# Performance work log

Measured on AMD Instinct MI355X. Metric: run time of the kernel, lower is better.

The kernel has to match this reference:

```python
import jax, jax.numpy as jnp
import numpy as np

B, S, H, KV, D, HID = 1, 2048, 32, 8, 128, 4096
SCALE = D ** -0.5
EPS = 1e-5
QMAX = 127.0  # 8-bit symmetric fake quant


def fake_quant(x):
    # per-tensor symmetric int8 fake quantization with straight-through estimator
    s = jnp.maximum(jnp.max(jnp.abs(x)), 1e-5) / QMAX
    q = jnp.clip(jnp.round(x / s), -QMAX - 1.0, QMAX) * s
    return x + jax.lax.stop_gradient(q - x)


def rms_norm(x, w):
    xf = x.astype(jnp.float32)
    var = jnp.mean(xf * xf, axis=-1, keepdims=True)
    return (xf * jax.lax.rsqrt(var + EPS)).astype(x.dtype) * w


def rotate_half(x):
    h = x.shape[-1] // 2
    return jnp.concatenate([-x[..., h:], x[..., :h]], axis=-1)


def qlinear(x, W):
    # QuantLinear: fake-quant activation and weight, then matmul (no bias)
    return fake_quant(x) @ fake_quant(W).T


def setup_inputs() -> dict:
    key = jax.random.key(0)
    ks = jax.random.split(key, 5)
    hidden_states = jax.random.normal(ks[0], (B, S, HID), jnp.float32)
    # RoPE tables
    inv_freq = 1.0 / (10000.0 ** (np.arange(0, D, 2, dtype=np.float32) / D))
    freqs = np.outer(np.arange(S, dtype=np.float32), inv_freq)  # [S, D/2]
    emb = np.concatenate([freqs, freqs], axis=-1)  # [S, D]
    cos = jnp.asarray(np.cos(emb))[None]  # [1,S,D]
    sin = jnp.asarray(np.sin(emb))[None]
    # causal additive mask [1,1,S,S]
    mask = jnp.where(np.tril(np.ones((S, S), dtype=bool)), 0.0, -1e9).astype(jnp.float32)[None, None]
    Wq = jax.random.normal(ks[1], (H * D, HID), jnp.float32) * 0.02
    Wk = jax.random.normal(ks[2], (KV * D, HID), jnp.float32) * 0.02
    Wv = jax.random.normal(ks[3], (KV * D, HID), jnp.float32) * 0.02
    Wo = jax.random.normal(ks[4], (HID, H * D), jnp.float32) * 0.02
    q_norm_w = jnp.ones((D,), jnp.float32)
    k_norm_w = jnp.ones((D,), jnp.float32)
    return dict(hidden_states=hidden_states, cos=cos, sin=sin, attention_mask=mask,
                Wq=Wq, Wk=Wk, Wv=Wv, Wo=Wo, q_norm_w=q_norm_w, k_norm_w=k_norm_w)


def reference(hidden_states, cos, sin, attention_mask, Wq, Wk, Wv, Wo, q_norm_w, k_norm_w):
    b, s, _ = hidden_states.shape
    q = qlinear(hidden_states, Wq).reshape(b, s, H, D).transpose(0, 2, 1, 3)   # [B,H,S,D]
    k = qlinear(hidden_states, Wk).reshape(b, s, KV, D).transpose(0, 2, 1, 3)  # [B,KV,S,D]
    v = qlinear(hidden_states, Wv).reshape(b, s, KV, D).transpose(0, 2, 1, 3)
    q = rms_norm(q, q_norm_w)
    k = rms_norm(k, k_norm_w)
    c = cos[:, None]  # unsqueeze head dim -> [1,1,S,D]
    sn = sin[:, None]
    q = q * c + rotate_half(q) * sn
    k = k * c + rotate_half(k) * sn
    n_rep = H // KV
    k = jnp.repeat(k, n_rep, axis=1)  # [B,H,S,D]
    v = jnp.repeat(v, n_rep, axis=1)
    # fake-quant around QK^T
    q = fake_quant(q)
    k = fake_quant(k)
    scores = jnp.einsum('bhqd,bhkd->bhqk', q, k) * SCALE + attention_mask
    p = jax.nn.softmax(scores.astype(jnp.float32), axis=-1).astype(q.dtype)
    # fake-quant around PV
    p = fake_quant(p)
    v = fake_quant(v)
    out = jnp.einsum('bhqk,bhkd->bhqd', p, v)
    out = out.transpose(0, 2, 1, 3).reshape(b, s, H * D)
    return qlinear(out, Wo)
```

## Files before the change

kernel.cpp:

```cpp
#include <hip/hip_runtime.h>
#include <hip/hip_bf16.h>
#include <math.h>
#include <stdint.h>

#define S_LEN 2048
#define NH    32
#define NKV   8
#define HD    128
#define HIDD  4096

typedef unsigned short u16;
typedef __attribute__((ext_vector_type(4))) int i32x4;

#define GLD16(g, l) __builtin_amdgcn_global_load_lds( \
    (const __attribute__((address_space(1))) void*)(g), \
    (__attribute__((address_space(3))) void*)(l), 16, 0, 0)


__device__ __forceinline__ float slot_scale(const unsigned* slot) {
    return fmaxf(__uint_as_float(*slot), 1e-5f) / 127.0f;
}

__device__ __forceinline__ int qint(float x, float s) {
    float q = rintf(x / s);
    q = fminf(fmaxf(q, -128.0f), 127.0f);
    return (int)q;
}

__device__ __forceinline__ void block_amax_atomic(float m, unsigned* slot) {
    __shared__ float wmax[8];
    const int lane = threadIdx.x & 63;
    const int wid  = threadIdx.x >> 6;
    const int nw   = blockDim.x >> 6;
    #pragma unroll
    for (int o = 32; o; o >>= 1) m = fmaxf(m, __shfl_xor(m, o));
    if (lane == 0) wmax[wid] = m;
    __syncthreads();
    if (threadIdx.x == 0) {
        float bm = wmax[0];
        for (int i = 1; i < nw; ++i) bm = fmaxf(bm, wmax[i]);
        atomicMax(slot, __float_as_uint(bm));
    }
}

struct Amax5Args { const float* p[5]; size_t n4[5]; };
__global__ __launch_bounds__(256) void absmax5_kernel(Amax5Args a, unsigned* slots) {
    const int t = blockIdx.y;
    const float4* x4 = (const float4*)a.p[t];
    const size_t n4 = a.n4[t];
    size_t i = (size_t)blockIdx.x * blockDim.x + threadIdx.x;
    size_t stride = (size_t)gridDim.x * blockDim.x;
    float m = 0.0f;
    for (; i < n4; i += stride) {
        float4 v = x4[i];
        m = fmaxf(m, fmaxf(fmaxf(fabsf(v.x), fabsf(v.y)), fmaxf(fabsf(v.z), fabsf(v.w))));
    }
    block_amax_atomic(m, slots + t);
}

struct Quant5Args { const float* p[5]; char* o[5]; size_t n4[5]; };
__global__ __launch_bounds__(256) void quant5_kernel(Quant5Args a, const unsigned* slots) {
    const int t = blockIdx.y;
    float s = slot_scale(slots + t);
    const float4* x4 = (const float4*)a.p[t];
    unsigned* o4 = (unsigned*)a.o[t];
    const size_t n4 = a.n4[t];
    size_t i = (size_t)blockIdx.x * blockDim.x + threadIdx.x;
    size_t stride = (size_t)gridDim.x * blockDim.x;
    for (; i < n4; i += stride) {
        float4 v = x4[i];
        unsigned o = (unsigned)(qint(v.x, s) & 255)
                   | ((unsigned)(qint(v.y, s) & 255) << 8)
                   | ((unsigned)(qint(v.z, s) & 255) << 16)
                   | ((unsigned)(qint(v.w, s) & 255) << 24);
        o4[i] = o;
    }
}

__global__ __launch_bounds__(256) void quant_kernel(const float* __restrict__ x,
                                                    size_t n4, const unsigned* slot,
                                                    char* __restrict__ out) {
    float s = slot_scale(slot);
    size_t i = (size_t)blockIdx.x * blockDim.x + threadIdx.x;
    size_t stride = (size_t)gridDim.x * blockDim.x;
    const float4* x4 = (const float4*)x;
    unsigned* o4 = (unsigned*)out;
    for (; i < n4; i += stride) {
        float4 v = x4[i];
        unsigned o = (unsigned)(qint(v.x, s) & 255)
                   | ((unsigned)(qint(v.y, s) & 255) << 8)
                   | ((unsigned)(qint(v.z, s) & 255) << 16)
                   | ((unsigned)(qint(v.w, s) & 255) << 24);
        o4[i] = o;
    }
}

__device__ __forceinline__ void gemm_body(const char* __restrict__ A,
                                          const char* __restrict__ B,
                                          float* __restrict__ C,
                                          int m0, int n0, int N, int K,
                                          float scale, unsigned* out_amax,
                                          char* Asm, char* Bsm) {
    const int tid  = threadIdx.x;
    const int lane = tid & 63;
    const int wave = tid >> 6;
    const int wr = (wave >> 1) * 64;
    const int wc = (wave & 1) * 64;
    const int l15 = lane & 15;
    const int l4  = lane >> 4;

    i32x4 acc[4][4];
    #pragma unroll
    for (int i = 0; i < 4; ++i)
        #pragma unroll
        for (int j = 0; j < 4; ++j) acc[i][j] = (i32x4){0, 0, 0, 0};

    for (int k0 = 0; k0 < K; k0 += 128) {
        __syncthreads();
        #pragma unroll
        for (int i = 0; i < 4; ++i) {
            int c2  = i * 256 + tid;
            int kk  = i >> 1;
            int row = (c2 >> 2) & 127;
            int col = (c2 & 3) * 16;
            GLD16(&A[(size_t)(m0 + row) * K + k0 + kk * 64 + col], &Asm[i * 4096 + wave * 1024]);
            GLD16(&B[(size_t)(n0 + row) * K + k0 + kk * 64 + col], &Bsm[i * 4096 + wave * 1024]);
        }
        __syncthreads();
        #pragma unroll
        for (int kk = 0; kk < 2; ++kk) {
            i32x4 af[4], bfr[4];
            #pragma unroll
            for (int i = 0; i < 4; ++i)
                af[i] = *(const i32x4*)&Asm[kk * 8192 + (wr + i * 16 + l15) * 64 + l4 * 16];
            #pragma unroll
            for (int j = 0; j < 4; ++j)
                bfr[j] = *(const i32x4*)&Bsm[kk * 8192 + (wc + j * 16 + l15) * 64 + l4 * 16];
            #pragma unroll
            for (int i = 0; i < 4; ++i)
                #pragma unroll
                for (int j = 0; j < 4; ++j)
                    acc[i][j] = __builtin_amdgcn_mfma_i32_16x16x64_i8(af[i], bfr[j], acc[i][j], 0, 0, 0);
        }
    }

    float lm = 0.0f;
    #pragma unroll
    for (int i = 0; i < 4; ++i)
        #pragma unroll
        for (int j = 0; j < 4; ++j)
            #pragma unroll
            for (int r = 0; r < 4; ++r) {
                int row = m0 + wr + i * 16 + l4 * 4 + r;
                int col = n0 + wc + j * 16 + l15;
                float v = (float)acc[i][j][r] * scale;
                C[(size_t)row * N + col] = v;
                lm = fmaxf(lm, fabsf(v));
            }
    if (out_amax) block_amax_atomic(lm, out_amax);
}

__global__ __launch_bounds__(256) void gemm_bt_kernel(const char* __restrict__ A,
                                                      const char* __restrict__ B,
                                                      float* __restrict__ C,
                                                      int N, int K,
                                                      const unsigned* __restrict__ sA_slot,
                                                      const unsigned* __restrict__ sB_slot,
                                                      unsigned* out_amax) {
    __shared__ __align__(16) char Asm[2 * 128 * 64];
    __shared__ __align__(16) char Bsm[2 * 128 * 64];
    int bid = blockIdx.y * 16 + blockIdx.x;
    int swz = (bid & 7) * 64 + (bid >> 3);
    float scale = slot_scale(sA_slot) * slot_scale(sB_slot);
    gemm_body(A, B, C, (swz & 15) * 128, (swz >> 4) * 128, N, K, scale, out_amax, Asm, Bsm);
}

__global__ __launch_bounds__(256) void gemm_kv_kernel(const char* __restrict__ A,
                                                      const char* __restrict__ Bk,
                                                      const char* __restrict__ Bv,
                                                      float* __restrict__ Ck,
                                                      float* __restrict__ Cv,
                                                      int K,
                                                      const unsigned* __restrict__ sA_slot,
                                                      const unsigned* __restrict__ sK_slot,
                                                      const unsigned* __restrict__ sV_slot,
                                                      unsigned* v_amax) {
    __shared__ __align__(16) char Asm[2 * 128 * 64];
    __shared__ __align__(16) char Bsm[2 * 128 * 64];
    int bid = blockIdx.y * 16 + blockIdx.x;
    int swz = (bid & 7) * 32 + (bid >> 3);
    int sx = swz & 15, sy = swz >> 4;
    const bool isv = sy >= 8;
    const char* B = isv ? Bv : Bk;
    float*      C = isv ? Cv : Ck;
    float scale = slot_scale(sA_slot) * slot_scale(isv ? sV_slot : sK_slot);
    gemm_body(A, B, C, sx * 128, (sy & 7) * 128, NKV * HD, K, scale,
              isv ? v_amax : nullptr, Asm, Bsm);
}

__global__ __launch_bounds__(256) void rmsrope2_kernel(float* __restrict__ qx,
                                                       float* __restrict__ kx,
                                                       const float* __restrict__ cosb,
                                                       const float* __restrict__ sinb,
                                                       const float* __restrict__ qw,
                                                       const float* __restrict__ kw,
                                                       unsigned* slots) {
    const int which = blockIdx.y;
    float* x = which ? kx : qx;
    const float* w = which ? kw : qw;
    const int s_shift = which ? 3 : 5;
    const int nrows = which ? (S_LEN * NKV) : (S_LEN * NH);
    unsigned* slot = slots + (which ? 6 : 5);

    const int lane = threadIdx.x & 63;
    const int wid  = threadIdx.x >> 6;
    const float wa = w[lane];
    const float wb = w[lane + 64];
    float lm = 0.0f;
    for (int row = blockIdx.x * 4 + wid; row < nrows; row += gridDim.x * 4) {
        int s = row >> s_shift;
        float* xr = x + (size_t)row * 128;
        float a = xr[lane], b = xr[lane + 64];
        float ss = a * a + b * b;
        #pragma unroll
        for (int o = 32; o; o >>= 1) ss += __shfl_xor(ss, o);
        float inv = 1.0f / sqrtf(ss * (1.0f / 128.0f) + 1e-5f);
        float ya = (a * inv) * wa;
        float yb = (b * inv) * wb;
        const float* cr = cosb + (size_t)s * 128;
        const float* sr = sinb + (size_t)s * 128;
        float o0 = ya * cr[lane]      - yb * sr[lane];
        float o1 = yb * cr[lane + 64] + ya * sr[lane + 64];
        xr[lane] = o0;
        xr[lane + 64] = o1;
        lm = fmaxf(lm, fmaxf(fabsf(o0), fabsf(o1)));
    }
    block_amax_atomic(lm, slot);
}

__global__ __launch_bounds__(256) void quant_qk2_kernel(const float* __restrict__ qx,
                                                        const float* __restrict__ kx,
                                                        const unsigned* slots,
                                                        char* __restrict__ qq,
                                                        char* __restrict__ kq) {
    int tid = blockIdx.x * 256 + threadIdx.x;
    const int qtot = S_LEN * NH * HD;
    if (tid < qtot) {
        float s = slot_scale(slots + 5);
        int d  = tid & 127;
        int h  = (tid >> 7) & 31;
        int sp = tid >> 12;
        qq[((size_t)h * S_LEN + sp) * 128 + d] = (char)qint(qx[tid], s);
    } else {
        tid -= qtot;
        float s = slot_scale(slots + 6);
        int d  = tid & 127;
        int h  = (tid >> 7) & 7;
        int sp = tid >> 10;
        kq[((size_t)h * S_LEN + sp) * 128 + d] = (char)qint(kx[tid], s);
    }
}

__global__ __launch_bounds__(256) void quant_v_kernel(const float* __restrict__ x,
                                                      const unsigned* slot,
                                                      char* __restrict__ out) {
    __shared__ unsigned char t8[64][36];
    const float s = slot_scale(slot);
    const int t   = threadIdx.x;
    const int sp0 = blockIdx.x * 64;
    const int d0  = blockIdx.y * 32;
    const int kvh = blockIdx.z;
    const int dl = t & 31;
    const int sb = t >> 5;
    #pragma unroll
    for (int j = 0; j < 8; ++j) {
        int spl = sb + j * 8;
        float v = x[((size_t)(sp0 + spl) * NKV + kvh) * 128 + d0 + dl];
        t8[spl][dl] = (unsigned char)qint(v, s);
    }
    __syncthreads();
    const int dd = t >> 3;
    const int ch = t & 7;
    unsigned lo = 0, hi = 0;
    #pragma unroll
    for (int j = 0; j < 4; ++j) lo |= (unsigned)t8[ch * 8 + j][dd] << (8 * j);
    #pragma unroll
    for (int j = 0; j < 4; ++j) hi |= (unsigned)t8[ch * 8 + 4 + j][dd] << (8 * j);
    *(uint2*)&out[((size_t)kvh * 128 + d0 + dd) * S_LEN + sp0 + ch * 8] = make_uint2(lo, hi);
}

__global__ __launch_bounds__(256) void attn_kernel(const char* __restrict__ Qq,
                                                   const char* __restrict__ Kq,
                                                   const char* __restrict__ Vt,
                                                   const unsigned* sq_slot,
                                                   const unsigned* sk_slot,
                                                   const unsigned* sv_slot,
                                                   float* __restrict__ O,
                                                   unsigned* amax_slot) {
    __shared__ __align__(16) char Klds[64 * 144];
    __shared__ __align__(16) char Vlds[128 * 80];
    __shared__ __align__(16) char plds[4][16 * 80];

    const int tid  = threadIdx.x;
    const int lane = tid & 63;
    const int wave = tid >> 6;
    const int h  = blockIdx.y;
    const int kv = h >> 2;
    const int l15 = lane & 15;
    const int l4  = lane >> 4;
    const size_t kvS = (size_t)kv * S_LEN;

    const float sq = slot_scale(sq_slot);
    const float sk = slot_scale(sk_slot);
    const float sv = slot_scale(sv_slot);
    const float qk_scale = sq * sk * 0.08838834764831845f;
    const float osc = (1.0f / 127.0f) * sv;
    const float NEG = -1e30f;

    float lm = 0.0f;

    #pragma unroll 1
    for (int tpass = 0; tpass < 2; ++tpass) {
        const int qt  = tpass ? (31 - (int)blockIdx.x) : (int)blockIdx.x;
        const int qr0 = qt * 64 + wave * 16;
        const int kb_last = qt * 4 + wave;
        const int nchunk  = qt + 1;

        i32x4 qf2[2];
        {
            const char* qp = Qq + ((size_t)h * S_LEN + qr0 + l15) * 128 + l4 * 16;
            qf2[0] = *(const i32x4*)(qp);
            qf2[1] = *(const i32x4*)(qp + 64);
        }

        float m_l = NEG, l_l = 0.0f;
        i32x4 kreg[2];
        #pragma unroll
        for (int c = 0; c < 2; ++c) {
            int idx = c * 256 + tid;
            kreg[c] = *(const i32x4*)&Kq[(kvS + (idx >> 3)) * 128 + (idx & 7) * 16];
        }
        #pragma unroll 1
        for (int kc = 0; kc < nchunk; ++kc) {
            __syncthreads();
            #pragma unroll
            for (int c = 0; c < 2; ++c) {
                int idx = c * 256 + tid;
                *(i32x4*)&Klds[(idx >> 3) * 144 + (idx & 7) * 16] = kreg[c];
            }
            __syncthreads();
            if (kc + 1 < nchunk) {
                #pragma unroll
                for (int c = 0; c < 2; ++c) {
                    int idx = c * 256 + tid;
                    kreg[c] = *(const i32x4*)&Kq[(kvS + (kc + 1) * 64 + (idx >> 3)) * 128 + (idx & 7) * 16];
                }
            }
            #pragma unroll
            for (int hb = 0; hb < 4; ++hb) {
                int kb = kc * 4 + hb;
                if (kb > kb_last) continue;
                i32x4 sacc = {0, 0, 0, 0};
                #pragma unroll
                for (int c = 0; c < 2; ++c) {
                    i32x4 kfa = *(const i32x4*)&Klds[(hb * 16 + l15) * 144 + c * 64 + l4 * 16];
                    sacc = __builtin_amdgcn_mfma_i32_16x16x64_i8(kfa, qf2[c], sacc, 0, 0, 0);
                }
                const bool diagb = (kb == kb_last);
                float sc[4];
                float bm = NEG;
                #pragma unroll
                for (int r = 0; r < 4; ++r) {
                    float x = (float)sacc[r] * qk_scale;
                    bool msk = diagb && ((l4 * 4 + r) > l15);
                    sc[r] = x;
                    bm = fmaxf(bm, msk ? NEG : x);
                }
                float mn = fmaxf(m_l, bm);
                float corr = __expf(m_l - mn);
                float ps = 0.0f;
                #pragma unroll
                for (int r = 0; r < 4; ++r) {
                    bool msk = diagb && ((l4 * 4 + r) > l15);
                    float p = msk ? 0.0f : __expf(sc[r] - mn);
                    ps += p;
                }
                l_l = l_l * corr + ps;
                m_l = mn;
            }
        }
        float m2 = fmaxf(m_l, __shfl_xor(m_l, 16));
        float mfin = fmaxf(m2, __shfl_xor(m2, 32));
        float t = l_l * __expf(m_l - mfin);
        t += __shfl_xor(t, 16);
        t += __shfl_xor(t, 32);
        float rl = 127.0f / t;
        float mrowB[4], rlB[4];
        #pragma unroll
        for (int r = 0; r < 4; ++r) {
            mrowB[r] = __shfl(mfin, l4 * 4 + r);
            rlB[r]   = __shfl(rl,   l4 * 4 + r);
        }

        i32x4 oacc[8];
        #pragma unroll
        for (int dt = 0; dt < 8; ++dt) oacc[dt] = (i32x4){0, 0, 0, 0};

        i32x4 vreg[2];
        #pragma unroll
        for (int c = 0; c < 2; ++c) {
            int idx = c * 256 + tid;
            kreg[c] = *(const i32x4*)&Kq[(kvS + (idx >> 3)) * 128 + (idx & 7) * 16];
            vreg[c] = *(const i32x4*)&Vt[((size_t)kv * 128 + (idx >> 2)) * S_LEN + (idx & 3) * 16];
        }
        #pragma unroll 1
        for (int kc = 0; kc < nchunk; ++kc) {
            __syncthreads();
            #pragma unroll
            for (int c = 0; c < 2; ++c) {
                int idx = c * 256 + tid;
                *(i32x4*)&Klds[(idx >> 3) * 144 + (idx & 7) * 16] = kreg[c];
                *(i32x4*)&Vlds[(idx >> 2) * 80 + (idx & 3) * 16] = vreg[c];
            }
            __syncthreads();
            if (kc + 1 < nchunk) {
                #pragma unroll
                for (int c = 0; c < 2; ++c) {
                    int idx = c * 256 + tid;
                    kreg[c] = *(const i32x4*)&Kq[(kvS + (kc + 1) * 64 + (idx >> 3)) * 128 + (idx & 7) * 16];
                    vreg[c] = *(const i32x4*)&Vt[((size_t)kv * 128 + (idx >> 2)) * S_LEN + (kc + 1) * 64 + (idx & 3) * 16];
                }
            }
            #pragma unroll
            for (int hb = 0; hb < 4; ++hb) {
                int kb = kc * 4 + hb;
                unsigned char pz[4] = {0, 0, 0, 0};
                if (kb <= kb_last) {
                    i32x4 sacc = {0, 0, 0, 0};
                    #pragma unroll
                    for (int c = 0; c < 2; ++c) {
                        i32x4 kfb = *(const i32x4*)&Klds[(hb * 16 + l15) * 144 + c * 64 + l4 * 16];
                        sacc = __builtin_amdgcn_mfma_i32_16x16x64_i8(qf2[c], kfb, sacc, 0, 0, 0);
                    }
                    const bool diagb = (kb == kb_last);
                    #pragma unroll
                    for (int r = 0; r < 4; ++r) {
                        float x = (float)sacc[r] * qk_scale;
                        float p = __expf(x - mrowB[r]) * rlB[r];
                        float pq = (diagb && (l15 > l4 * 4 + r)) ? 0.0f : rintf(p);
                        pz[r] = (unsigned char)(int)pq;
                    }
                }
                #pragma unroll
                for (int r = 0; r < 4; ++r)
                    plds[wave][(l4 * 4 + r) * 80 + hb * 16 + l15] = pz[r];
            }
            i32x4 pf = *(const i32x4*)&plds[wave][l15 * 80 + l4 * 16];
            #pragma unroll
            for (int dt = 0; dt < 8; ++dt) {
                i32x4 vfb = *(const i32x4*)&Vlds[(dt * 16 + l15) * 80 + l4 * 16];
                oacc[dt] = __builtin_amdgcn_mfma_i32_16x16x64_i8(pf, vfb, oacc[dt], 0, 0, 0);
            }
        }

        #pragma unroll
        for (int dt = 0; dt < 8; ++dt)
            #pragma unroll
            for (int r = 0; r < 4; ++r) {
                int qrow = qr0 + l4 * 4 + r;
                float v = (float)oacc[dt][r] * osc;
                O[(size_t)qrow * (NH * 128) + h * 128 + dt * 16 + l15] = v;
                lm = fmaxf(lm, fabsf(v));
            }
    }
    block_amax_atomic(lm, amax_slot);
}

extern "C" void kernel_launch(void* const* d_in, const int* in_sizes, int n_in,
                              void* d_out, int out_size, void* d_ws, size_t ws_size,
                              hipStream_t stream) {
    const float* hs   = (const float*)d_in[0];
    const float* cosb = (const float*)d_in[1];
    const float* sinb = (const float*)d_in[2];
    const float* Wq   = (const float*)d_in[4];
    const float* Wk   = (const float*)d_in[5];
    const float* Wv   = (const float*)d_in[6];
    const float* Wo   = (const float*)d_in[7];
    const float* qnw  = (const float*)d_in[8];
    const float* knw  = (const float*)d_in[9];
    float* out = (float*)d_out;

    char* ws = (char*)d_ws;
    unsigned* slots = (unsigned*)ws;
    size_t off = 256;
    auto take = [&](size_t bytes) { size_t o = off; off += (bytes + 255) & ~(size_t)255; return o; };
    char*  hsq  = (char*)(ws + take((size_t)S_LEN * HIDD));
    char*  Wqq  = (char*)(ws + take((size_t)NH * HD * HIDD));
    char*  Wkq  = (char*)(ws + take((size_t)NKV * HD * HIDD));
    char*  Wvq  = (char*)(ws + take((size_t)NKV * HD * HIDD));
    char*  Woq  = (char*)(ws + take((size_t)HIDD * NH * HD));
    float* qf   = (float*)(ws + take((size_t)S_LEN * NH * HD * 4));
    float* kf   = (float*)(ws + take((size_t)S_LEN * NKV * HD * 4));
    float* vf   = (float*)(ws + take((size_t)S_LEN * NKV * HD * 4));
    char*  qq   = (char*)(ws + take((size_t)NH * S_LEN * HD));
    char*  kq   = (char*)(ws + take((size_t)NKV * S_LEN * HD));
    char*  vtq  = (char*)(ws + take((size_t)NKV * HD * S_LEN));
    float* attnf = qf;
    char*  attnq = hsq;

    hipMemsetAsync(ws, 0, 64, stream);

    const size_t n_hs = (size_t)S_LEN * HIDD;
    const size_t n_wq = (size_t)NH * HD * HIDD;
    const size_t n_wk = (size_t)NKV * HD * HIDD;

    Amax5Args aa;
    aa.p[0] = hs; aa.p[1] = Wq; aa.p[2] = Wk; aa.p[3] = Wv; aa.p[4] = Wo;
    aa.n4[0] = n_hs / 4; aa.n4[1] = n_wq / 4; aa.n4[2] = n_wk / 4;
    aa.n4[3] = n_wk / 4; aa.n4[4] = n_wq / 4;
    absmax5_kernel<<<dim3(512, 5), 256, 0, stream>>>(aa, slots);

    Quant5Args qa;
    qa.p[0] = hs; qa.p[1] = Wq; qa.p[2] = Wk; qa.p[3] = Wv; qa.p[4] = Wo;
    qa.o[0] = hsq; qa.o[1] = Wqq; qa.o[2] = Wkq; qa.o[3] = Wvq; qa.o[4] = Woq;
    qa.n4[0] = n_hs / 4; qa.n4[1] = n_wq / 4; qa.n4[2] = n_wk / 4;
    qa.n4[3] = n_wk / 4; qa.n4[4] = n_wq / 4;
    quant5_kernel<<<dim3(1024, 5), 256, 0, stream>>>(qa, slots);

    gemm_bt_kernel<<<dim3(16, 32), 256, 0, stream>>>(hsq, Wqq, qf, NH * HD, HIDD,
                                                     slots + 0, slots + 1, nullptr);
    gemm_kv_kernel<<<dim3(16, 16), 256, 0, stream>>>(hsq, Wkq, Wvq, kf, vf, HIDD,
                                                     slots + 0, slots + 2, slots + 3, slots + 7);

    rmsrope2_kernel<<<dim3(1024, 2), 256, 0, stream>>>(qf, kf, cosb, sinb, qnw, knw, slots);

    quant_qk2_kernel<<<40960, 256, 0, stream>>>(qf, kf, slots, qq, kq);
    quant_v_kernel<<<dim3(32, 4, 8), 256, 0, stream>>>(vf, slots + 7, vtq);

    attn_kernel<<<dim3(16, NH), 256, 0, stream>>>(qq, kq, vtq,
                                                  slots + 5, slots + 6, slots + 7,
                                                  attnf, slots + 8);

    quant_kernel<<<2048, 256, 0, stream>>>(attnf, n_hs / 4, slots + 8, attnq);
    gemm_bt_kernel<<<dim3(16, 32), 256, 0, stream>>>(attnq, Woq, out, NH * HD, HIDD,
                                                     slots + 8, slots + 4, nullptr);
    (void)in_sizes; (void)n_in; (void)out_size; (void)ws_size;
}
```

Baseline: 388.9 us.

## Double-buffer int8 GEMM with swizzled LDS, merge QKV GEMMs, split attention tiles

The int8 GEMM body now double-buffers 64-wide K tiles, issuing the next global-to-LDS load before the current tile's MFMAs, and XOR-swizzles LDS columns to cut bank conflicts. The Q, K and V projections are merged into one 768-block launch, and the O projection gets its own kernel. The attention kernel drops its two-pass pairing of a short and a long causal tile per block, launching 32x32 blocks of one tile each. It also computes S^T so probabilities can be packed to LDS as 32-bit words instead of byte stores. Launch count and pipeline stalls should drop, but the causal tiles are now imbalanced across blocks.

```diff
diff --git a/kernel.cpp b/kernel.cpp
--- a/kernel.cpp
+++ b/kernel.cpp
@@ -108,6 +108,9 @@
     const int wc = (wave & 1) * 64;
     const int l15 = lane & 15;
     const int l4  = lane >> 4;
+    const int cx  = (l4 ^ (l15 & 3)) * 16;
+    const int r0  = tid >> 2;
+    const int sc  = ((tid & 3) ^ ((tid >> 2) & 3)) * 16;
 
     i32x4 acc[4][4];
     #pragma unroll
@@ -115,33 +118,33 @@
         #pragma unroll
         for (int j = 0; j < 4; ++j) acc[i][j] = (i32x4){0, 0, 0, 0};
 
-    for (int k0 = 0; k0 < K; k0 += 128) {
+    auto STAGE = [&](int buf, int k0) {
+        GLD16(&A[(size_t)(m0 + r0) * K + k0 + sc],      &Asm[buf * 8192 + wave * 1024]);
+        GLD16(&A[(size_t)(m0 + 64 + r0) * K + k0 + sc], &Asm[buf * 8192 + 4096 + wave * 1024]);
+        GLD16(&B[(size_t)(n0 + r0) * K + k0 + sc],      &Bsm[buf * 8192 + wave * 1024]);
+        GLD16(&B[(size_t)(n0 + 64 + r0) * K + k0 + sc], &Bsm[buf * 8192 + 4096 + wave * 1024]);
+    };
+
+    STAGE(0, 0);
+    __syncthreads();
+    int cur = 0;
+    const int NT = K >> 6;
+    for (int t = 0; t < NT; ++t) {
+        if (t + 1 < NT) STAGE(cur ^ 1, (t + 1) << 6);
+        i32x4 af[4], bfr[4];
+        #pragma unroll
+        for (int i = 0; i < 4; ++i)
+            af[i] = *(const i32x4*)&Asm[cur * 8192 + (wr + i * 16 + l15) * 64 + cx];
+        #pragma unroll
+        for (int j = 0; j < 4; ++j)
+            bfr[j] = *(const i32x4*)&Bsm[cur * 8192 + (wc + j * 16 + l15) * 64 + cx];
+        #pragma unroll
+        for (int i = 0; i < 4; ++i)
+            #pragma unroll
+            for (int j = 0; j < 4; ++j)
+                acc[i][j] = __builtin_amdgcn_mfma_i32_16x16x64_i8(af[i], bfr[j], acc[i][j], 0, 0, 0);
         __syncthreads();
-        #pragma unroll
-        for (int i = 0; i < 4; ++i) {
-            int c2  = i * 256 + tid;
-            int kk  = i >> 1;
-            int row = (c2 >> 2) & 127;
-            int col = (c2 & 3) * 16;
-            GLD16(&A[(size_t)(m0 + row) * K + k0 + kk * 64 + col], &Asm[i * 4096 + wave * 1024]);
-            GLD16(&B[(size_t)(n0 + row) * K + k0 + kk * 64 + col], &Bsm[i * 4096 + wave * 1024]);
-        }
-        __syncthreads();
-        #pragma unroll
-        for (int kk = 0; kk < 2; ++kk) {
-            i32x4 af[4], bfr[4];
-            #pragma unroll
-            for (int i = 0; i < 4; ++i)
-                af[i] = *(const i32x4*)&Asm[kk * 8192 + (wr + i * 16 + l15) * 64 + l4 * 16];
-            #pragma unroll
-            for (int j = 0; j < 4; ++j)
-                bfr[j] = *(const i32x4*)&Bsm[kk * 8192 + (wc + j * 16 + l15) * 64 + l4 * 16];
-            #pragma unroll
-            for (int i = 0; i < 4; ++i)
-                #pragma unroll
-                for (int j = 0; j < 4; ++j)
-                    acc[i][j] = __builtin_amdgcn_mfma_i32_16x16x64_i8(af[i], bfr[j], acc[i][j], 0, 0, 0);
-        }
+        cur ^= 1;
     }
 
     float lm = 0.0f;
@@ -160,42 +163,39 @@
     if (out_amax) block_amax_atomic(lm, out_amax);
 }
 
-__global__ __launch_bounds__(256) void gemm_bt_kernel(const char* __restrict__ A,
-                                                      const char* __restrict__ B,
-                                                      float* __restrict__ C,
-                                                      int N, int K,
-                                                      const unsigned* __restrict__ sA_slot,
-                                                      const unsigned* __restrict__ sB_slot,
-                                                      unsigned* out_amax) {
-    __shared__ __align__(16) char Asm[2 * 128 * 64];
-    __shared__ __align__(16) char Bsm[2 * 128 * 64];
-    int bid = blockIdx.y * 16 + blockIdx.x;
+__global__ __launch_bounds__(256) void gemm_qkv_kernel(const char* __restrict__ Aq,
+                                                       const char* __restrict__ Wqq,
+                                                       const char* __restrict__ Wkq,
+                                                       const char* __restrict__ Wvq,
+                                                       float* __restrict__ qf,
+                                                       float* __restrict__ kf,
+                                                       float* __restrict__ vf,
+                                                       const unsigned* __restrict__ slots,
+                                                       unsigned* v_amax) {
+    __shared__ __align__(16) char Asm[2 * 8192];
+    __shared__ __align__(16) char Bsm[2 * 8192];
+    int bid = blockIdx.x;
+    int swz = (bid & 7) * 96 + (bid >> 3);
+    int x = swz & 15, y = swz >> 4;
+    const char* B; float* C; int N, nb; const unsigned* sB; unsigned* am = nullptr;
+    if (y < 32)      { B = Wqq; C = qf; N = NH * HD;  nb = y;      sB = slots + 1; }
+    else if (y < 40) { B = Wkq; C = kf; N = NKV * HD; nb = y - 32; sB = slots + 2; }
+    else             { B = Wvq; C = vf; N = NKV * HD; nb = y - 40; sB = slots + 3; am = v_amax; }
+    float scale = slot_scale(slots + 0) * slot_scale(sB);
+    gemm_body(Aq, B, C, x * 128, nb * 128, N, HIDD, scale, am, Asm, Bsm);
+}
+
+__global__ __launch_bounds__(256) void gemm_o_kernel(const char* __restrict__ A,
+                                                     const char* __restrict__ Woq,
+                                                     float* __restrict__ C,
+                                                     const unsigned* __restrict__ slots) {
+    __shared__ __align__(16) char Asm[2 * 8192];
+    __shared__ __align__(16) char Bsm[2 * 8192];
+    int bid = blockIdx.x;
     int swz = (bid & 7) * 64 + (bid >> 3);
-    float scale = slot_scale(sA_slot) * slot_scale(sB_slot);
-    gemm_body(A, B, C, (swz & 15) * 128, (swz >> 4) * 128, N, K, scale, out_amax, Asm, Bsm);
-}
-
-__global__ __launch_bounds__(256) void gemm_kv_kernel(const char* __restrict__ A,
-                                                      const char* __restrict__ Bk,
-                                                      const char* __restrict__ Bv,
-                                                      float* __restrict__ Ck,
-                                                      float* __restrict__ Cv,
-                                                      int K,
-                                                      const unsigned* __restrict__ sA_slot,
-                                                      const unsigned* __restrict__ sK_slot,
-                                                      const unsigned* __restrict__ sV_slot,
-                                                      unsigned* v_amax) {
-    __shared__ __align__(16) char Asm[2 * 128 * 64];
-    __shared__ __align__(16) char Bsm[2 * 128 * 64];
-    int bid = blockIdx.y * 16 + blockIdx.x;
-    int swz = (bid & 7) * 32 + (bid >> 3);
-    int sx = swz & 15, sy = swz >> 4;
-    const bool isv = sy >= 8;
-    const char* B = isv ? Bv : Bk;
-    float*      C = isv ? Cv : Ck;
-    float scale = slot_scale(sA_slot) * slot_scale(isv ? sV_slot : sK_slot);
-    gemm_body(A, B, C, sx * 128, (sy & 7) * 128, NKV * HD, K, scale,
-              isv ? v_amax : nullptr, Asm, Bsm);
+    int x = swz & 15, y = swz >> 4;
+    float scale = slot_scale(slots + 8) * slot_scale(slots + 4);
+    gemm_body(A, Woq, C, x * 128, y * 128, NH * HD, HIDD, scale, nullptr, Asm, Bsm);
 }
 
 __global__ __launch_bounds__(256) void rmsrope2_kernel(float* __restrict__ qx,
@@ -310,6 +310,11 @@
     const int l4  = lane >> 4;
     const size_t kvS = (size_t)kv * S_LEN;
 
+    const int qt  = 31 - (int)blockIdx.x;
+    const int qr0 = qt * 64 + wave * 16;
+    const int kb_last = qt * 4 + wave;
+    const int nchunk  = qt + 1;
+
     const float sq = slot_scale(sq_slot);
     const float sk = slot_scale(sk_slot);
     const float sv = slot_scale(sv_slot);
@@ -317,49 +322,110 @@
     const float osc = (1.0f / 127.0f) * sv;
     const float NEG = -1e30f;
 
-    float lm = 0.0f;
-
+    i32x4 qf2[2];
+    {
+        const char* qp = Qq + ((size_t)h * S_LEN + qr0 + l15) * 128 + l4 * 16;
+        qf2[0] = *(const i32x4*)(qp);
+        qf2[1] = *(const i32x4*)(qp + 64);
+    }
+
+    float m_l = NEG, l_l = 0.0f;
+    i32x4 kreg[2];
+    #pragma unroll
+    for (int c = 0; c < 2; ++c) {
+        int idx = c * 256 + tid;
+        kreg[c] = *(const i32x4*)&Kq[(kvS + (idx >> 3)) * 128 + (idx & 7) * 16];
+    }
     #pragma unroll 1
-    for (int tpass = 0; tpass < 2; ++tpass) {
-        const int qt  = tpass ? (31 - (int)blockIdx.x) : (int)blockIdx.x;
-        const int qr0 = qt * 64 + wave * 16;
-        const int kb_last = qt * 4 + wave;
-        const int nchunk  = qt + 1;
-
-        i32x4 qf2[2];
-        {
-            const char* qp = Qq + ((size_t)h * S_LEN + qr0 + l15) * 128 + l4 * 16;
-            qf2[0] = *(const i32x4*)(qp);
-            qf2[1] = *(const i32x4*)(qp + 64);
-        }
-
-        float m_l = NEG, l_l = 0.0f;
-        i32x4 kreg[2];
+    for (int kc = 0; kc < nchunk; ++kc) {
+        __syncthreads();
         #pragma unroll
         for (int c = 0; c < 2; ++c) {
             int idx = c * 256 + tid;
-            kreg[c] = *(const i32x4*)&Kq[(kvS + (idx >> 3)) * 128 + (idx & 7) * 16];
-        }
-        #pragma unroll 1
-        for (int kc = 0; kc < nchunk; ++kc) {
-            __syncthreads();
+            *(i32x4*)&Klds[(idx >> 3) * 144 + (idx & 7) * 16] = kreg[c];
+        }
+        __syncthreads();
+        if (kc + 1 < nchunk) {
             #pragma unroll
             for (int c = 0; c < 2; ++c) {
                 int idx = c * 256 + tid;
-                *(i32x4*)&Klds[(idx >> 3) * 144 + (idx & 7) * 16] = kreg[c];
-            }
-            __syncthreads();
-            if (kc + 1 < nchunk) {
-                #pragma unroll
-                for (int c = 0; c < 2; ++c) {
-                    int idx = c * 256 + tid;
-                    kreg[c] = *(const i32x4*)&Kq[(kvS + (kc + 1) * 64 + (idx >> 3)) * 128 + (idx & 7) * 16];
-                }
-            }
-            #pragma unroll
-            for (int hb = 0; hb < 4; ++hb) {
-                int kb = kc * 4 + hb;
-                if (kb > kb_last) continue;
+                kreg[c] = *(const i32x4*)&Kq[(kvS + (kc + 1) * 64 + (idx >> 3)) * 128 + (idx & 7) * 16];
+            }
+        }
+        #pragma unroll
+        for (int hb = 0; hb < 4; ++hb) {
+            int kb = kc * 4 + hb;
+            if (kb > kb_last) continue;
+            i32x4 sacc = {0, 0, 0, 0};
+            #pragma unroll
+            for (int c = 0; c < 2; ++c) {
+                i32x4 kfa = *(const i32x4*)&Klds[(hb * 16 + l15) * 144 + c * 64 + l4 * 16];
+                sacc = __builtin_amdgcn_mfma_i32_16x16x64_i8(kfa, qf2[c], sacc, 0, 0, 0);
+            }
+            const bool diagb = (kb == kb_last);
+            float sc[4];
+            float bm = NEG;
+            #pragma unroll
+            for (int r = 0; r < 4; ++r) {
+                float x = (float)sacc[r] * qk_scale;
+                bool msk = diagb && ((l4 * 4 + r) > l15);
+                sc[r] = x;
+                bm = fmaxf(bm, msk ? NEG : x);
+            }
+            float mn = fmaxf(m_l, bm);
+            float corr = __expf(m_l - mn);
+            float ps = 0.0f;
+            #pragma unroll
+            for (int r = 0; r < 4; ++r) {
+                bool msk = diagb && ((l4 * 4 + r) > l15);
+                float p = msk ? 0.0f : __expf(sc[r] - mn);
+                ps += p;
+            }
+            l_l = l_l * corr + ps;
+            m_l = mn;
+        }
+    }
+    float m2 = fmaxf(m_l, __shfl_xor(m_l, 16));
+    float mfin = fmaxf(m2, __shfl_xor(m2, 32));
+    float t = l_l * __expf(m_l - mfin);
+    t += __shfl_xor(t, 16);
+    t += __shfl_xor(t, 32);
+    float rl = 127.0f / t;
+
+    i32x4 oacc[8];
+    #pragma unroll
+    for (int dt = 0; dt < 8; ++dt) oacc[dt] = (i32x4){0, 0, 0, 0};
+
+    i32x4 vreg[2];
+    #pragma unroll
+    for (int c = 0; c < 2; ++c) {
+        int idx = c * 256 + tid;
+        kreg[c] = *(const i32x4*)&Kq[(kvS + (idx >> 3)) * 128 + (idx & 7) * 16];
+        vreg[c] = *(const i32x4*)&Vt[((size_t)kv * 128 + (idx >> 2)) * S_LEN + (idx & 3) * 16];
+    }
+    #pragma unroll 1
+    for (int kc = 0; kc < nchunk; ++kc) {
+        __syncthreads();
+        #pragma unroll
+        for (int c = 0; c < 2; ++c) {
+            int idx = c * 256 + tid;
+            *(i32x4*)&Klds[(idx >> 3) * 144 + (idx & 7) * 16] = kreg[c];
+            *(i32x4*)&Vlds[(idx >> 2) * 80 + (idx & 3) * 16] = vreg[c];
+        }
+        __syncthreads();
+        if (kc + 1 < nchunk) {
+            #pragma unroll
+            for (int c = 0; c < 2; ++c) {
+                int idx = c * 256 + tid;
+                kreg[c] = *(const i32x4*)&Kq[(kvS + (kc + 1) * 64 + (idx >> 3)) * 128 + (idx & 7) * 16];
+                vreg[c] = *(const i32x4*)&Vt[((size_t)kv * 128 + (idx >> 2)) * S_LEN + (kc + 1) * 64 + (idx & 3) * 16];
+            }
+        }
+        #pragma unroll
+        for (int hb = 0; hb < 4; ++hb) {
+            int kb = kc * 4 + hb;
+            unsigned pack = 0;
+            if (kb <= kb_last) {
                 i32x4 sacc = {0, 0, 0, 0};
                 #pragma unroll
                 for (int c = 0; c < 2; ++c) {
@@ -367,112 +433,34 @@
                     sacc = __builtin_amdgcn_mfma_i32_16x16x64_i8(kfa, qf2[c], sacc, 0, 0, 0);
                 }
                 const bool diagb = (kb == kb_last);
-                float sc[4];
-                float bm = NEG;
                 #pragma unroll
                 for (int r = 0; r < 4; ++r) {
                     float x = (float)sacc[r] * qk_scale;
-                    bool msk = diagb && ((l4 * 4 + r) > l15);
-                    sc[r] = x;
-                    bm = fmaxf(bm, msk ? NEG : x);
+                    float p = __expf(x - mfin) * rl;
+                    float pq = (diagb && ((l4 * 4 + r) > l15)) ? 0.0f : rintf(p);
+                    pack |= ((unsigned)(int)pq) << (8 * r);
                 }
-                float mn = fmaxf(m_l, bm);
-                float corr = __expf(m_l - mn);
-                float ps = 0.0f;
-                #pragma unroll
-                for (int r = 0; r < 4; ++r) {
-                    bool msk = diagb && ((l4 * 4 + r) > l15);
-                    float p = msk ? 0.0f : __expf(sc[r] - mn);
-                    ps += p;
-                }
-                l_l = l_l * corr + ps;
-                m_l = mn;
-            }
-        }
-        float m2 = fmaxf(m_l, __shfl_xor(m_l, 16));
-        float mfin = fmaxf(m2, __shfl_xor(m2, 32));
-        float t = l_l * __expf(m_l - mfin);
-        t += __shfl_xor(t, 16);
-        t += __shfl_xor(t, 32);
-        float rl = 127.0f / t;
-        float mrowB[4], rlB[4];
+            }
+            *(unsigned*)&plds[wave][l15 * 80 + hb * 16 + l4 * 4] = pack;
+        }
+        i32x4 pf = *(const i32x4*)&plds[wave][l15 * 80 + l4 * 16];
+        #pragma unroll
+        for (int dt = 0; dt < 8; ++dt) {
+            i32x4 vfb = *(const i32x4*)&Vlds[(dt * 16 + l15) * 80 + l4 * 16];
+            oacc[dt] = __builtin_amdgcn_mfma_i32_16x16x64_i8(pf, vfb, oacc[dt], 0, 0, 0);
+        }
+    }
+
+    float lm = 0.0f;
+    #pragma unroll
+    for (int dt = 0; dt < 8; ++dt)
         #pragma unroll
         for (int r = 0; r < 4; ++r) {
-            mrowB[r] = __shfl(mfin, l4 * 4 + r);
-            rlB[r]   = __shfl(rl,   l4 * 4 + r);
-        }
-
-        i32x4 oacc[8];
-        #pragma unroll
-        for (int dt = 0; dt < 8; ++dt) oacc[dt] = (i32x4){0, 0, 0, 0};
-
-        i32x4 vreg[2];
-        #pragma unroll
-        for (int c = 0; c < 2; ++c) {
-            int idx = c * 256 + tid;
-            kreg[c] = *(const i32x4*)&Kq[(kvS + (idx >> 3)) * 128 + (idx & 7) * 16];
-            vreg[c] = *(const i32x4*)&Vt[((size_t)kv * 128 + (idx >> 2)) * S_LEN + (idx & 3) * 16];
-        }
-        #pragma unroll 1
-        for (int kc = 0; kc < nchunk; ++kc) {
-            __syncthreads();
-            #pragma unroll
-            for (int c = 0; c < 2; ++c) {
-                int idx = c * 256 + tid;
-                *(i32x4*)&Klds[(idx >> 3) * 144 + (idx & 7) * 16] = kreg[c];
-                *(i32x4*)&Vlds[(idx >> 2) * 80 + (idx & 3) * 16] = vreg[c];
-            }
-            __syncthreads();
-            if (kc + 1 < nchunk) {
-                #pragma unroll
-                for (int c = 0; c < 2; ++c) {
-                    int idx = c * 256 + tid;
-                    kreg[c] = *(const i32x4*)&Kq[(kvS + (kc + 1) * 64 + (idx >> 3)) * 128 + (idx & 7) * 16];
-                    vreg[c] = *(const i32x4*)&Vt[((size_t)kv * 128 + (idx >> 2)) * S_LEN + (kc + 1) * 64 + (idx & 3) * 16];
-                }
-            }
-            #pragma unroll
-            for (int hb = 0; hb < 4; ++hb) {
-                int kb = kc * 4 + hb;
-                unsigned char pz[4] = {0, 0, 0, 0};
-                if (kb <= kb_last) {
-                    i32x4 sacc = {0, 0, 0, 0};
-                    #pragma unroll
-                    for (int c = 0; c < 2; ++c) {
-                        i32x4 kfb = *(const i32x4*)&Klds[(hb * 16 + l15) * 144 + c * 64 + l4 * 16];
-                        sacc = __builtin_amdgcn_mfma_i32_16x16x64_i8(qf2[c], kfb, sacc, 0, 0, 0);
-                    }
-                    const bool diagb = (kb == kb_last);
-                    #pragma unroll
-                    for (int r = 0; r < 4; ++r) {
-                        float x = (float)sacc[r] * qk_scale;
-                        float p = __expf(x - mrowB[r]) * rlB[r];
-                        float pq = (diagb && (l15 > l4 * 4 + r)) ? 0.0f : rintf(p);
-                        pz[r] = (unsigned char)(int)pq;
-                    }
-                }
-                #pragma unroll
-                for (int r = 0; r < 4; ++r)
-                    plds[wave][(l4 * 4 + r) * 80 + hb * 16 + l15] = pz[r];
-            }
-            i32x4 pf = *(const i32x4*)&plds[wave][l15 * 80 + l4 * 16];
-            #pragma unroll
-            for (int dt = 0; dt < 8; ++dt) {
-                i32x4 vfb = *(const i32x4*)&Vlds[(dt * 16 + l15) * 80 + l4 * 16];
-                oacc[dt] = __builtin_amdgcn_mfma_i32_16x16x64_i8(pf, vfb, oacc[dt], 0, 0, 0);
-            }
-        }
-
-        #pragma unroll
-        for (int dt = 0; dt < 8; ++dt)
-            #pragma unroll
-            for (int r = 0; r < 4; ++r) {
-                int qrow = qr0 + l4 * 4 + r;
-                float v = (float)oacc[dt][r] * osc;
-                O[(size_t)qrow * (NH * 128) + h * 128 + dt * 16 + l15] = v;
-                lm = fmaxf(lm, fabsf(v));
-            }
-    }
+            int qrow = qr0 + l4 * 4 + r;
+            float v = (float)oacc[dt][r] * osc;
+            O[(size_t)qrow * (NH * 128) + h * 128 + dt * 16 + l15] = v;
+            lm = fmaxf(lm, fabsf(v));
+        }
     block_amax_atomic(lm, amax_slot);
 }
 
@@ -527,22 +515,19 @@
     qa.n4[3] = n_wk / 4; qa.n4[4] = n_wq / 4;
     quant5_kernel<<<dim3(1024, 5), 256, 0, stream>>>(qa, slots);
 
-    gemm_bt_kernel<<<dim3(16, 32), 256, 0, stream>>>(hsq, Wqq, qf, NH * HD, HIDD,
-                                                     slots + 0, slots + 1, nullptr);
-    gemm_kv_kernel<<<dim3(16, 16), 256, 0, stream>>>(hsq, Wkq, Wvq, kf, vf, HIDD,
-                                                     slots + 0, slots + 2, slots + 3, slots + 7);
+    gemm_qkv_kernel<<<768, 256, 0, stream>>>(hsq, Wqq, Wkq, Wvq, qf, kf, vf,
+                                             slots, slots + 7);
 
     rmsrope2_kernel<<<dim3(1024, 2), 256, 0, stream>>>(qf, kf, cosb, sinb, qnw, knw, slots);
 
     quant_qk2_kernel<<<40960, 256, 0, stream>>>(qf, kf, slots, qq, kq);
     quant_v_kernel<<<dim3(32, 4, 8), 256, 0, stream>>>(vf, slots + 7, vtq);
 
-    attn_kernel<<<dim3(16, NH), 256, 0, stream>>>(qq, kq, vtq,
+    attn_kernel<<<dim3(32, NH), 256, 0, stream>>>(qq, kq, vtq,
                                                   slots + 5, slots + 6, slots + 7,
                                                   attnf, slots + 8);
 
     quant_kernel<<<2048, 256, 0, stream>>>(attnf, n_hs / 4, slots + 8, attnq);
-    gemm_bt_kernel<<<dim3(16, 32), 256, 0, stream>>>(attnq, Woq, out, NH * HD, HIDD,
-                                                     slots + 8, slots + 4, nullptr);
+    gemm_o_kernel<<<512, 256, 0, stream>>>(attnq, Woq, out, slots);
     (void)in_sizes; (void)n_in; (void)out_size; (void)ws_size;
 }
```

Result: slower. 410.0 us (+5.4%).
